# Kernel tuning notes

Hardware: AMD Instinct MI355X
Metric: run time of the kernel (lower is better)

## Reference

```python
import jax, jax.numpy as jnp
import numpy as np

HIDDEN = 128
HEADS = 4
S = 128          # number of scenes
N = 64           # pedestrians per scene
TOTAL = S * N


def setup_inputs() -> dict:
    key = jax.random.key(0)
    ks = jax.random.split(key, 12)
    h = HIDDEN
    return {
        "node_features": jax.random.normal(ks[0], (TOTAL, h), jnp.float32),
        "positions": jax.random.normal(ks[1], (TOTAL, 2), jnp.float32),
        # rel_pos_encoder: Linear(2, h//2) -> ReLU -> Linear(h//2, h)
        "W1": jax.random.normal(ks[2], (h // 2, 2), jnp.float32) * 0.5,
        "b1": jax.random.normal(ks[3], (h // 2,), jnp.float32) * 0.02,
        "W2": jax.random.normal(ks[4], (h, h // 2), jnp.float32) * (1.0 / np.sqrt(h // 2)),
        "b2": jax.random.normal(ks[5], (h,), jnp.float32) * 0.02,
        # MultiheadAttention packed in-projection (q,k,v stacked) and out-projection
        "in_proj_w": jax.random.normal(ks[6], (3 * h, h), jnp.float32) * (1.0 / np.sqrt(h)),
        "in_proj_b": jax.random.normal(ks[7], (3 * h,), jnp.float32) * 0.02,
        "out_w": jax.random.normal(ks[8], (h, h), jnp.float32) * (1.0 / np.sqrt(h)),
        "out_b": jax.random.normal(ks[9], (h,), jnp.float32) * 0.02,
        # output_proj: Linear(2h, h)
        "proj_w": jax.random.normal(ks[10], (h, 2 * h), jnp.float32) * (1.0 / np.sqrt(2 * h)),
        "proj_b": jax.random.normal(ks[11], (h,), jnp.float32) * 0.02,
        "num_scenes": S,
        "peds_per_scene": N,
    }


def reference(node_features, positions, W1, b1, W2, b2,
              in_proj_w, in_proj_b, out_w, out_b, proj_w, proj_b,
              num_scenes, peds_per_scene):
    h = node_features.shape[-1]
    heads = HEADS
    dh = h // heads
    s, n = num_scenes, peds_per_scene

    feats = node_features.reshape(s, n, h)          # (S, n, h)
    pos = positions.reshape(s, n, 2)                # (S, n, 2)

    # rel[s, i, j] = pos[j] - pos[i]  (matches unsqueeze(0) - unsqueeze(1))
    rel = pos[:, None, :, :] - pos[:, :, None, :]   # (S, n, n, 2)
    rel_enc = jnp.maximum(rel @ W1.T + b1, 0.0) @ W2.T + b2  # (S, n, n, h)

    Wq, Wk, Wv = jnp.split(in_proj_w, 3, axis=0)
    bq, bk, bv = jnp.split(in_proj_b, 3, axis=0)

    # query: each ped i attends over keys j = feats[j] + rel_enc[i, j]
    key_in = feats[:, None, :, :] + rel_enc          # (S, n, n, h)
    q = (feats @ Wq.T + bq).reshape(s, n, heads, dh)             # (S, n, H, dh)
    k = (key_in @ Wk.T + bk).reshape(s, n, n, heads, dh)         # (S, n, n, H, dh)
    v = (key_in @ Wv.T + bv).reshape(s, n, n, heads, dh)

    scores = jnp.einsum('sihd,sijhd->shij', q, k) / np.sqrt(dh)  # (S, H, n, n)
    attn = jax.nn.softmax(scores, axis=-1)
    ctx = jnp.einsum('shij,sijhd->sihd', attn, v).reshape(s, n, h)
    attn_out = ctx @ out_w.T + out_b                              # (S, n, h)

    combined = jnp.concatenate([feats, attn_out], axis=-1)       # (S, n, 2h)
    out = combined @ proj_w.T + proj_b                            # (S, n, h)
    return out.reshape(s * n, h)
```

## Files before the change

### kernel.cpp

```cpp
#include <hip/hip_runtime.h>
#include <hip/hip_bf16.h>


typedef unsigned int u32;
#define SCALE 0.17677669529663689f

__device__ __forceinline__ float bl(u32 u){ union{u32 x; float f;} c; c.x = u << 16; return c.f; }
__device__ __forceinline__ float bh(u32 u){ union{u32 x; float f;} c; c.x = u & 0xffff0000u; return c.f; }
__device__ __forceinline__ u32 pk(float a, float b){
  union{float f; u32 x;} ca, cb; ca.f = a; cb.f = b;
  u32 ua = (ca.x + 0x7fffu + ((ca.x >> 16) & 1u)) >> 16;
  u32 ub = (cb.x + 0x7fffu + ((cb.x >> 16) & 1u)) >> 16;
  return ua | (ub << 16);
}
__device__ __forceinline__ float dot8(uint4 u, float4 f0, float4 f1, float acc){
  acc = fmaf(bl(u.x), f0.x, acc); acc = fmaf(bh(u.x), f0.y, acc);
  acc = fmaf(bl(u.y), f0.z, acc); acc = fmaf(bh(u.y), f0.w, acc);
  acc = fmaf(bl(u.z), f1.x, acc); acc = fmaf(bh(u.z), f1.y, acc);
  acc = fmaf(bl(u.w), f1.z, acc); acc = fmaf(bh(u.w), f1.w, acc);
  return acc;
}
__device__ __forceinline__ void wsync(){
  __builtin_amdgcn_s_waitcnt(0xC07F);
  __builtin_amdgcn_wave_barrier();
}

__global__ __launch_bounds__(256, 2) void ee_setup(
    const float* __restrict__ nf, const float* __restrict__ b2,
    const float* __restrict__ ipw, const float* __restrict__ ipb,
    const float* __restrict__ w2,
    const float* __restrict__ ow, const float* __restrict__ pw,
    float* __restrict__ W2KT, float* __restrict__ W2VT,
    u32* __restrict__ WQB, u32* __restrict__ OWB, u32* __restrict__ PWB,
    u32* __restrict__ KBt, u32* __restrict__ VB)
{
  const int tid = threadIdx.x, b = blockIdx.x;
  const int cg = tid >> 6, l = tid & 63;
  const float2* ipw2 = (const float2*)ipw;
  const float2* ow2  = (const float2*)ow;
  const float2* pw2  = (const float2*)pw;

  if (b >= 544) {
    for (int k = 0; k < 16; ++k) {
      int i = (b - 544) * 4096 + k * 256 + tid;
      if (i < 8192)       { float2 f = ipw2[i];        WQB[i]        = pk(f.x, f.y); }
      else if (i < 16384) { float2 f = ow2[i - 8192];  OWB[i - 8192] = pk(f.x, f.y); }
      else                { float2 f = pw2[i - 16384]; PWB[i - 16384]= pk(f.x, f.y); }
    }
    return;
  }
  if (b >= 512) {
    int t = (b - 512) * 4 + cg;
    int kv = t & 1, e = t >> 1;
    int c0 = 2 * l;
    const float4* rp = (const float4*)ipw + (size_t)(128 + kv * 128 + c0) * 32;
    const float* w2e = w2 + __builtin_amdgcn_readfirstlane(e);
    float a0 = 0.f, a1 = 0.f;
    #pragma unroll 8
    for (int c4 = 0; c4 < 32; ++c4) {
      float4 wa = rp[c4], wb = rp[32 + c4];
      float x0 = w2e[(4 * c4 + 0) * 64];
      float x1 = w2e[(4 * c4 + 1) * 64];
      float x2 = w2e[(4 * c4 + 2) * 64];
      float x3 = w2e[(4 * c4 + 3) * 64];
      a0 = fmaf(wa.x, x0, a0); a0 = fmaf(wa.y, x1, a0);
      a0 = fmaf(wa.z, x2, a0); a0 = fmaf(wa.w, x3, a0);
      a1 = fmaf(wb.x, x0, a1); a1 = fmaf(wb.y, x1, a1);
      a1 = fmaf(wb.z, x2, a1); a1 = fmaf(wb.w, x3, a1);
    }
    float* dst = kv ? W2VT : W2KT;
    ((float2*)dst)[e * 64 + l] = make_float2(a0, a1);
    return;
  }

  const int s = b >> 2, kv = (b >> 1) & 1, hlf = b & 1;
  __shared__ __align__(16) u32 fbS[64][68];
  __shared__ u32 vtS[64][33];
  const float2* nf2 = (const float2*)nf;
  const float2* b22 = (const float2*)b2;

  for (int idx = tid; idx < 4096; idx += 256) {
    int j = idx >> 6, mw = idx & 63;
    float2 f = nf2[((s << 6) + j) * 64 + mw];
    float2 bb = b22[mw];
    fbS[j][mw] = pk(f.x + bb.x, f.y + bb.y);
  }
  __syncthreads();

  uint4 fr[16];
  {
    const uint4* frow = (const uint4*)&fbS[l][0];
    #pragma unroll
    for (int k = 0; k < 16; ++k) fr[k] = frow[k];
  }
  #pragma unroll 1
  for (int p = 0; p < 8; ++p) {
    int c0 = hlf * 64 + cg * 16 + 2 * p;
    int r0 = 128 + kv * 128 + c0;
    const float4* w0 = (const float4*)ipw +
                       (size_t)__builtin_amdgcn_readfirstlane(r0) * 32;
    const float4* w1r = w0 + 32;
    float a0 = ipb[r0], a1 = ipb[r0 + 1];
    #pragma unroll
    for (int k = 0; k < 16; ++k) {
      uint4 F = fr[k];
      float4 wa = w0[2 * k],  wb = w0[2 * k + 1];
      float4 xa = w1r[2 * k], xb = w1r[2 * k + 1];
      float e0 = bl(F.x), e1 = bh(F.x), e2 = bl(F.y), e3 = bh(F.y);
      float e4 = bl(F.z), e5 = bh(F.z), e6 = bl(F.w), e7 = bh(F.w);
      a0 = fmaf(e0, wa.x, a0); a0 = fmaf(e1, wa.y, a0);
      a0 = fmaf(e2, wa.z, a0); a0 = fmaf(e3, wa.w, a0);
      a0 = fmaf(e4, wb.x, a0); a0 = fmaf(e5, wb.y, a0);
      a0 = fmaf(e6, wb.z, a0); a0 = fmaf(e7, wb.w, a0);
      a1 = fmaf(e0, xa.x, a1); a1 = fmaf(e1, xa.y, a1);
      a1 = fmaf(e2, xa.z, a1); a1 = fmaf(e3, xa.w, a1);
      a1 = fmaf(e4, xb.x, a1); a1 = fmaf(e5, xb.y, a1);
      a1 = fmaf(e6, xb.z, a1); a1 = fmaf(e7, xb.w, a1);
    }
    u32 v = pk(a0, a1);
    int cw = hlf * 32 + cg * 8 + p;
    if (kv == 0) KBt[(((s << 6) + cw) << 6) + l] = v;
    else         vtS[l][cg * 8 + p] = v;
  }
  if (kv == 1) {
    __syncthreads();
    int r = tid >> 2, cb = (tid & 3) * 8;
    #pragma unroll
    for (int k = 0; k < 8; ++k)
      VB[(((s << 6) + r) << 6) + hlf * 32 + cb + k] = vtS[r][cb + k];
  }
}

__global__ __launch_bounds__(256, 2) void ee_main(
    const float* __restrict__ nf, const float* __restrict__ pos,
    const float* __restrict__ w1, const float* __restrict__ b1,
    const float* __restrict__ ipb,
    const float* __restrict__ ob, const float* __restrict__ pb,
    const float* __restrict__ W2KT, const float* __restrict__ W2VT,
    const u32* __restrict__ WQB, const u32* __restrict__ OWB,
    const u32* __restrict__ PWB,
    const u32* __restrict__ KBt, const u32* __restrict__ VB,
    float* __restrict__ outp)
{
  __shared__ __align__(16) float pxS[64], pyS[64], w1xS[64], w1yS[64], b1S[64];
  __shared__ __align__(16) float fqS[4][4][132];
  __shared__ __align__(16) float qS [4][4][132];
  __shared__ __align__(16) float qwS[4][4][4][68];
  __shared__ __align__(16) float atS[4][4][4][68];
  __shared__ __align__(16) float whS[4][4][4][68];

  const int tid = threadIdx.x;
  const int s = blockIdx.x >> 2, qt = blockIdx.x & 3;
  const int w = tid >> 6, l = tid & 63;
  const int c0 = 2 * l;

  if (tid < 64) {
    float2 p = ((const float2*)pos)[(s << 6) + tid];
    pxS[tid] = p.x; pyS[tid] = p.y;
    float2 wv = ((const float2*)w1)[tid];
    w1xS[tid] = wv.x; w1yS[tid] = wv.y;
    b1S[tid] = b1[tid];
  }
  __syncthreads();

  int il[4], ig[4];
  #pragma unroll
  for (int t = 0; t < 4; ++t) { il[t] = qt * 16 + 4 * w + t; ig[t] = (s << 6) + il[t]; }

  #pragma unroll
  for (int t = 0; t < 4; ++t)
    *(float2*)&fqS[w][t][c0] = ((const float2*)nf)[ig[t] * 64 + l];
  wsync();

  {
    float2 bq = ((const float2*)ipb)[l];
    float a0[4], a1[4];
    #pragma unroll
    for (int t = 0; t < 4; ++t) { a0[t] = bq.x; a1[t] = bq.y; }
    const uint4* W4 = (const uint4*)WQB;
    #pragma unroll 4
    for (int m8 = 0; m8 < 16; ++m8) {
      uint4 ua = W4[c0 * 16 + m8];
      uint4 ub = W4[(c0 + 1) * 16 + m8];
      #pragma unroll
      for (int t = 0; t < 4; ++t) {
        float4 f0 = *(const float4*)&fqS[w][t][8 * m8];
        float4 f1 = *(const float4*)&fqS[w][t][8 * m8 + 4];
        a0[t] = dot8(ua, f0, f1, a0[t]);
        a1[t] = dot8(ub, f0, f1, a1[t]);
      }
    }
    #pragma unroll
    for (int t = 0; t < 4; ++t)
      *(float2*)&qS[w][t][c0] = make_float2(a0[t], a1[t]);
  }
  wsync();

  {
    const float4* G4 = (const float4*)W2KT;
    #pragma unroll
    for (int hd = 0; hd < 4; ++hd) {
      float acc[4] = {0.f, 0.f, 0.f, 0.f};
      #pragma unroll
      for (int dq = 0; dq < 8; ++dq) {
        float4 g = G4[l * 32 + hd * 8 + dq];
        #pragma unroll
        for (int t = 0; t < 4; ++t) {
          float4 qf = *(const float4*)&qS[w][t][hd * 32 + 4 * dq];
          acc[t] = fmaf(g.x, qf.x, acc[t]); acc[t] = fmaf(g.y, qf.y, acc[t]);
          acc[t] = fmaf(g.z, qf.z, acc[t]); acc[t] = fmaf(g.w, qf.w, acc[t]);
        }
      }
      #pragma unroll
      for (int t = 0; t < 4; ++t) qwS[w][t][hd][l] = acc[t];
    }
  }
  wsync();

  float at[4][4];
  float pix[4], piy[4];
  {
    float pjx = pxS[l], pjy = pyS[l];
    float rx[4], ry[4];
    #pragma unroll
    for (int t = 0; t < 4; ++t) {
      pix[t] = pxS[il[t]]; piy[t] = pyS[il[t]];
      rx[t] = pjx - pix[t]; ry[t] = pjy - piy[t];
    }
    float sc[4][4];
    #pragma unroll
    for (int t = 0; t < 4; ++t)
      #pragma unroll
      for (int hd = 0; hd < 4; ++hd) sc[t][hd] = 0.f;

    const u32* kbp = KBt + (s << 12);
    #pragma unroll 8
    for (int m2 = 0; m2 < 32; ++m2) {
      u32 u0 = kbp[((2 * m2) << 6) + l];
      u32 u1 = kbp[((2 * m2 + 1) << 6) + l];
      const int hd = m2 >> 3;
      #pragma unroll
      for (int t = 0; t < 4; ++t) {
        float4 qf = *(const float4*)&qS[w][t][4 * m2];
        sc[t][hd] = fmaf(bl(u0), qf.x, sc[t][hd]);
        sc[t][hd] = fmaf(bh(u0), qf.y, sc[t][hd]);
        sc[t][hd] = fmaf(bl(u1), qf.z, sc[t][hd]);
        sc[t][hd] = fmaf(bh(u1), qf.w, sc[t][hd]);
      }
    }
    #pragma unroll 2
    for (int eb = 0; eb < 8; ++eb) {
      float4 wx0 = *(const float4*)&w1xS[8 * eb];
      float4 wx1 = *(const float4*)&w1xS[8 * eb + 4];
      float4 wy0 = *(const float4*)&w1yS[8 * eb];
      float4 wy1 = *(const float4*)&w1yS[8 * eb + 4];
      float4 bb0 = *(const float4*)&b1S[8 * eb];
      float4 bb1 = *(const float4*)&b1S[8 * eb + 4];
      #pragma unroll
      for (int t = 0; t < 4; ++t) {
        float h0 = fmaxf(0.f, fmaf(rx[t], wx0.x, fmaf(ry[t], wy0.x, bb0.x)));
        float h1 = fmaxf(0.f, fmaf(rx[t], wx0.y, fmaf(ry[t], wy0.y, bb0.y)));
        float h2 = fmaxf(0.f, fmaf(rx[t], wx0.z, fmaf(ry[t], wy0.z, bb0.z)));
        float h3 = fmaxf(0.f, fmaf(rx[t], wx0.w, fmaf(ry[t], wy0.w, bb0.w)));
        float h4 = fmaxf(0.f, fmaf(rx[t], wx1.x, fmaf(ry[t], wy1.x, bb1.x)));
        float h5 = fmaxf(0.f, fmaf(rx[t], wx1.y, fmaf(ry[t], wy1.y, bb1.y)));
        float h6 = fmaxf(0.f, fmaf(rx[t], wx1.z, fmaf(ry[t], wy1.z, bb1.z)));
        float h7 = fmaxf(0.f, fmaf(rx[t], wx1.w, fmaf(ry[t], wy1.w, bb1.w)));
        #pragma unroll
        for (int hd = 0; hd < 4; ++hd) {
          float4 q0 = *(const float4*)&qwS[w][t][hd][8 * eb];
          float4 q1 = *(const float4*)&qwS[w][t][hd][8 * eb + 4];
          float a = sc[t][hd];
          a = fmaf(q0.x, h0, a); a = fmaf(q0.y, h1, a);
          a = fmaf(q0.z, h2, a); a = fmaf(q0.w, h3, a);
          a = fmaf(q1.x, h4, a); a = fmaf(q1.y, h5, a);
          a = fmaf(q1.z, h6, a); a = fmaf(q1.w, h7, a);
          sc[t][hd] = a;
        }
      }
    }
    #pragma unroll
    for (int t = 0; t < 4; ++t) {
      #pragma unroll
      for (int hd = 0; hd < 4; ++hd) {
        float v = sc[t][hd] * SCALE;
        float m = v;
        #pragma unroll
        for (int off = 32; off > 0; off >>= 1) m = fmaxf(m, __shfl_xor(m, off));
        float p = __expf(v - m);
        float su = p;
        #pragma unroll
        for (int off = 32; off > 0; off >>= 1) su += __shfl_xor(su, off);
#if __has_builtin(__builtin_amdgcn_rcpf)
        at[t][hd] = p * __builtin_amdgcn_rcpf(su);
#else
        at[t][hd] = p / su;
#endif
        atS[w][t][hd][l] = at[t][hd];
      }
    }
  }
  wsync();

  {
    float wx = w1xS[l], wy = w1yS[l], bb = b1S[l];
    float wh[4][4];
    #pragma unroll
    for (int t = 0; t < 4; ++t)
      #pragma unroll
      for (int hd = 0; hd < 4; ++hd) wh[t][hd] = 0.f;
    #pragma unroll 4
    for (int j4 = 0; j4 < 16; ++j4) {
      float4 px = *(const float4*)&pxS[4 * j4];
      float4 py = *(const float4*)&pyS[4 * j4];
      #pragma unroll
      for (int t = 0; t < 4; ++t) {
        float4 a0v = *(const float4*)&atS[w][t][0][4 * j4];
        float4 a1v = *(const float4*)&atS[w][t][1][4 * j4];
        float4 a2v = *(const float4*)&atS[w][t][2][4 * j4];
        float4 a3v = *(const float4*)&atS[w][t][3][4 * j4];
        float h;
        h = fmaxf(0.f, fmaf(px.x - pix[t], wx, fmaf(py.x - piy[t], wy, bb)));
        wh[t][0] = fmaf(a0v.x, h, wh[t][0]); wh[t][1] = fmaf(a1v.x, h, wh[t][1]);
        wh[t][2] = fmaf(a2v.x, h, wh[t][2]); wh[t][3] = fmaf(a3v.x, h, wh[t][3]);
        h = fmaxf(0.f, fmaf(px.y - pix[t], wx, fmaf(py.y - piy[t], wy, bb)));
        wh[t][0] = fmaf(a0v.y, h, wh[t][0]); wh[t][1] = fmaf(a1v.y, h, wh[t][1]);
        wh[t][2] = fmaf(a2v.y, h, wh[t][2]); wh[t][3] = fmaf(a3v.y, h, wh[t][3]);
        h = fmaxf(0.f, fmaf(px.z - pix[t], wx, fmaf(py.z - piy[t], wy, bb)));
        wh[t][0] = fmaf(a0v.z, h, wh[t][0]); wh[t][1] = fmaf(a1v.z, h, wh[t][1]);
        wh[t][2] = fmaf(a2v.z, h, wh[t][2]); wh[t][3] = fmaf(a3v.z, h, wh[t][3]);
        h = fmaxf(0.f, fmaf(px.w - pix[t], wx, fmaf(py.w - piy[t], wy, bb)));
        wh[t][0] = fmaf(a0v.w, h, wh[t][0]); wh[t][1] = fmaf(a1v.w, h, wh[t][1]);
        wh[t][2] = fmaf(a2v.w, h, wh[t][2]); wh[t][3] = fmaf(a3v.w, h, wh[t][3]);
      }
    }
    #pragma unroll
    for (int t = 0; t < 4; ++t)
      #pragma unroll
      for (int hd = 0; hd < 4; ++hd) whS[w][t][hd][l] = wh[t][hd];
  }
  wsync();

  {
    const int hd = l >> 4;
    float cx0[4] = {0,0,0,0}, cx1[4] = {0,0,0,0};
    const float2* V2 = (const float2*)W2VT;
    const u32* vbp = VB + (s << 12);
    #pragma unroll 4
    for (int n4 = 0; n4 < 16; ++n4) {
      float2 g0 = V2[((4 * n4 + 0) << 6) + l];
      float2 g1 = V2[((4 * n4 + 1) << 6) + l];
      float2 g2 = V2[((4 * n4 + 2) << 6) + l];
      float2 g3 = V2[((4 * n4 + 3) << 6) + l];
      u32 v0 = vbp[((4 * n4 + 0) << 6) + l];
      u32 v1 = vbp[((4 * n4 + 1) << 6) + l];
      u32 v2 = vbp[((4 * n4 + 2) << 6) + l];
      u32 v3 = vbp[((4 * n4 + 3) << 6) + l];
      #pragma unroll
      for (int t = 0; t < 4; ++t) {
        float4 whv = *(const float4*)&whS[w][t][hd][4 * n4];
        float4 atv = *(const float4*)&atS[w][t][hd][4 * n4];
        float a0 = cx0[t], a1 = cx1[t];
        a0 = fmaf(whv.x, g0.x, a0); a1 = fmaf(whv.x, g0.y, a1);
        a0 = fmaf(atv.x, bl(v0), a0); a1 = fmaf(atv.x, bh(v0), a1);
        a0 = fmaf(whv.y, g1.x, a0); a1 = fmaf(whv.y, g1.y, a1);
        a0 = fmaf(atv.y, bl(v1), a0); a1 = fmaf(atv.y, bh(v1), a1);
        a0 = fmaf(whv.z, g2.x, a0); a1 = fmaf(whv.z, g2.y, a1);
        a0 = fmaf(atv.z, bl(v2), a0); a1 = fmaf(atv.z, bh(v2), a1);
        a0 = fmaf(whv.w, g3.x, a0); a1 = fmaf(whv.w, g3.y, a1);
        a0 = fmaf(atv.w, bl(v3), a0); a1 = fmaf(atv.w, bh(v3), a1);
        cx0[t] = a0; cx1[t] = a1;
      }
    }
    wsync();
    #pragma unroll
    for (int t = 0; t < 4; ++t)
      *(float2*)&qS[w][t][c0] = make_float2(cx0[t], cx1[t]);
  }
  wsync();

  {
    float2 b = ((const float2*)ob)[l];
    float a0[4], a1[4];
    #pragma unroll
    for (int t = 0; t < 4; ++t) { a0[t] = b.x; a1[t] = b.y; }
    const uint4* W4 = (const uint4*)OWB;
    #pragma unroll 4
    for (int m8 = 0; m8 < 16; ++m8) {
      uint4 ua = W4[c0 * 16 + m8];
      uint4 ub = W4[(c0 + 1) * 16 + m8];
      #pragma unroll
      for (int t = 0; t < 4; ++t) {
        float4 f0 = *(const float4*)&qS[w][t][8 * m8];
        float4 f1 = *(const float4*)&qS[w][t][8 * m8 + 4];
        a0[t] = dot8(ua, f0, f1, a0[t]);
        a1[t] = dot8(ub, f0, f1, a1[t]);
      }
    }
    wsync();
    #pragma unroll
    for (int t = 0; t < 4; ++t)
      *(float2*)(&whS[w][t][0][0] + c0) = make_float2(a0[t], a1[t]);
  }
  wsync();

  {
    float2 b = ((const float2*)pb)[l];
    float a0[4], a1[4];
    #pragma unroll
    for (int t = 0; t < 4; ++t) { a0[t] = b.x; a1[t] = b.y; }
    const uint4* W4 = (const uint4*)PWB;
    #pragma unroll 2
    for (int m8 = 0; m8 < 16; ++m8) {
      uint4 ua = W4[c0 * 32 + m8];
      uint4 ub = W4[(c0 + 1) * 32 + m8];
      uint4 uc = W4[c0 * 32 + 16 + m8];
      uint4 ud = W4[(c0 + 1) * 32 + 16 + m8];
      #pragma unroll
      for (int t = 0; t < 4; ++t) {
        float4 f0 = *(const float4*)&fqS[w][t][8 * m8];
        float4 f1 = *(const float4*)&fqS[w][t][8 * m8 + 4];
        float4 g0 = *(const float4*)(&whS[w][t][0][0] + 8 * m8);
        float4 g1 = *(const float4*)(&whS[w][t][0][0] + 8 * m8 + 4);
        a0[t] = dot8(ua, f0, f1, a0[t]);
        a1[t] = dot8(ub, f0, f1, a1[t]);
        a0[t] = dot8(uc, g0, g1, a0[t]);
        a1[t] = dot8(ud, g0, g1, a1[t]);
      }
    }
    #pragma unroll
    for (int t = 0; t < 4; ++t)
      ((float2*)outp)[ig[t] * 64 + l] = make_float2(a0[t], a1[t]);
  }
}

extern "C" void kernel_launch(void* const* d_in, const int* in_sizes, int n_in,
                              void* d_out, int out_size, void* d_ws, size_t ws_size,
                              hipStream_t stream) {
  (void)in_sizes; (void)n_in; (void)out_size; (void)ws_size;
  const float* nf  = (const float*)d_in[0];
  const float* pos = (const float*)d_in[1];
  const float* w1  = (const float*)d_in[2];
  const float* b1  = (const float*)d_in[3];
  const float* w2  = (const float*)d_in[4];
  const float* b2  = (const float*)d_in[5];
  const float* ipw = (const float*)d_in[6];
  const float* ipb = (const float*)d_in[7];
  const float* ow  = (const float*)d_in[8];
  const float* ob  = (const float*)d_in[9];
  const float* pw  = (const float*)d_in[10];
  const float* pb  = (const float*)d_in[11];

  char* ws = (char*)d_ws;
  float* W2KT = (float*)(ws);
  float* W2VT = (float*)(ws + (32 << 10));
  u32* WQB  = (u32*)(ws + (64 << 10));
  u32* OWB  = (u32*)(ws + (96 << 10));
  u32* PWB  = (u32*)(ws + (128 << 10));
  u32* KBt  = (u32*)(ws + (192 << 10));
  u32* VB   = (u32*)(ws + (192 << 10) + (128 * 4096 * 4));

  ee_setup<<<dim3(552), dim3(256), 0, stream>>>(nf, b2, ipw, ipb, w2, ow, pw,
                                                W2KT, W2VT, WQB, OWB, PWB, KBt, VB);
  ee_main<<<dim3(512), dim3(256), 0, stream>>>(nf, pos, w1, b1, ipb, ob, pb,
                                               W2KT, W2VT, WQB, OWB, PWB,
                                               KBt, VB, (float*)d_out);
}
```

Baseline: 174.5 us.

## Move Q projection and feature half of output projection into setup kernel

The setup kernel now also computes the Q projection (fp32, stored to a workspace buffer) and the node-feature half of the output projection (written directly into the output as a partial sum), doubling its per-scene block count. The main kernel drops its Q GEMV and the feature half of the final projection, reading Q from global memory and accumulating onto the partial output. This shortens the main kernel's serial chain but adds global traffic for Q and the partial result, plus more setup blocks.

```diff
diff --git a/kernel.cpp b/kernel.cpp
--- a/kernel.cpp
+++ b/kernel.cpp
@@ -29,28 +29,32 @@
     const float* __restrict__ nf, const float* __restrict__ b2,
     const float* __restrict__ ipw, const float* __restrict__ ipb,
     const float* __restrict__ w2,
-    const float* __restrict__ ow, const float* __restrict__ pw,
+    const float* __restrict__ pw, const float* __restrict__ pb,
+    const float* __restrict__ ow,
     float* __restrict__ W2KT, float* __restrict__ W2VT,
-    u32* __restrict__ WQB, u32* __restrict__ OWB, u32* __restrict__ PWB,
-    u32* __restrict__ KBt, u32* __restrict__ VB)
+    u32* __restrict__ OWB, u32* __restrict__ PW2B,
+    u32* __restrict__ KBt, u32* __restrict__ VB,
+    float* __restrict__ QB, float* __restrict__ PF)
 {
   const int tid = threadIdx.x, b = blockIdx.x;
   const int cg = tid >> 6, l = tid & 63;
-  const float2* ipw2 = (const float2*)ipw;
-  const float2* ow2  = (const float2*)ow;
-  const float2* pw2  = (const float2*)pw;
-
-  if (b >= 544) {
+
+  if (b >= 1056) {
+    const float2* ow2 = (const float2*)ow;
+    const float2* pw2 = (const float2*)pw;
     for (int k = 0; k < 16; ++k) {
-      int i = (b - 544) * 4096 + k * 256 + tid;
-      if (i < 8192)       { float2 f = ipw2[i];        WQB[i]        = pk(f.x, f.y); }
-      else if (i < 16384) { float2 f = ow2[i - 8192];  OWB[i - 8192] = pk(f.x, f.y); }
-      else                { float2 f = pw2[i - 16384]; PWB[i - 16384]= pk(f.x, f.y); }
+      int i = (b - 1056) * 4096 + k * 256 + tid;
+      if (i < 8192) { float2 f = ow2[i]; OWB[i] = pk(f.x, f.y); }
+      else {
+        int m = i - 8192; int c = m >> 6, mw = m & 63;
+        float2 f = pw2[c * 128 + 64 + mw];
+        PW2B[m] = pk(f.x, f.y);
+      }
     }
     return;
   }
-  if (b >= 512) {
-    int t = (b - 512) * 4 + cg;
+  if (b >= 1024) {
+    int t = (b - 1024) * 4 + cg;
     int kv = t & 1, e = t >> 1;
     int c0 = 2 * l;
     const float4* rp = (const float4*)ipw + (size_t)(128 + kv * 128 + c0) * 32;
@@ -73,17 +77,17 @@
     return;
   }
 
-  const int s = b >> 2, kv = (b >> 1) & 1, hlf = b & 1;
+  const int s = b >> 3, mat = (b >> 1) & 3, hlf = b & 1;
   __shared__ __align__(16) u32 fbS[64][68];
-  __shared__ u32 vtS[64][33];
+  __shared__ __align__(16) u32 xS[64][68];
   const float2* nf2 = (const float2*)nf;
   const float2* b22 = (const float2*)b2;
 
   for (int idx = tid; idx < 4096; idx += 256) {
     int j = idx >> 6, mw = idx & 63;
     float2 f = nf2[((s << 6) + j) * 64 + mw];
-    float2 bb = b22[mw];
-    fbS[j][mw] = pk(f.x + bb.x, f.y + bb.y);
+    if (mat < 2) { float2 bb = b22[mw]; f.x += bb.x; f.y += bb.y; }
+    fbS[j][mw] = pk(f.x, f.y);
   }
   __syncthreads();
 
@@ -93,14 +97,18 @@
     #pragma unroll
     for (int k = 0; k < 16; ++k) fr[k] = frow[k];
   }
+  const float* wbase = (mat == 3) ? pw : ipw;
+  const int rbase = (mat == 0) ? 128 : (mat == 1) ? 256 : 0;
+  const int rlen4 = (mat == 3) ? 64 : 32;
+  const float* bptr = (mat == 3) ? pb : (ipb + rbase);
+
   #pragma unroll 1
   for (int p = 0; p < 8; ++p) {
     int c0 = hlf * 64 + cg * 16 + 2 * p;
-    int r0 = 128 + kv * 128 + c0;
-    const float4* w0 = (const float4*)ipw +
-                       (size_t)__builtin_amdgcn_readfirstlane(r0) * 32;
-    const float4* w1r = w0 + 32;
-    float a0 = ipb[r0], a1 = ipb[r0 + 1];
+    int row = __builtin_amdgcn_readfirstlane(rbase + c0);
+    const float4* w0 = (const float4*)wbase + (size_t)row * rlen4;
+    const float4* w1r = w0 + rlen4;
+    float a0 = bptr[c0], a1 = bptr[c0 + 1];
     #pragma unroll
     for (int k = 0; k < 16; ++k) {
       uint4 F = fr[k];
@@ -117,37 +125,48 @@
       a1 = fmaf(e4, xb.x, a1); a1 = fmaf(e5, xb.y, a1);
       a1 = fmaf(e6, xb.z, a1); a1 = fmaf(e7, xb.w, a1);
     }
-    u32 v = pk(a0, a1);
-    int cw = hlf * 32 + cg * 8 + p;
-    if (kv == 0) KBt[(((s << 6) + cw) << 6) + l] = v;
-    else         vtS[l][cg * 8 + p] = v;
-  }
-  if (kv == 1) {
+    if (mat == 0) {
+      KBt[(((s << 6) + hlf * 32 + cg * 8 + p) << 6) + l] = pk(a0, a1);
+    } else if (mat == 1) {
+      xS[l][cg * 8 + p] = pk(a0, a1);
+    } else {
+      float* fx = (float*)xS;
+      fx[l * 68 + cg * 16 + 2 * p]     = a0;
+      fx[l * 68 + cg * 16 + 2 * p + 1] = a1;
+    }
+  }
+  if (mat == 1) {
     __syncthreads();
     int r = tid >> 2, cb = (tid & 3) * 8;
     #pragma unroll
     for (int k = 0; k < 8; ++k)
-      VB[(((s << 6) + r) << 6) + hlf * 32 + cb + k] = vtS[r][cb + k];
+      VB[(((s << 6) + r) << 6) + hlf * 32 + cb + k] = xS[r][cb + k];
+  } else if (mat >= 2) {
+    __syncthreads();
+    int r = tid >> 2, g = (tid & 3) * 16;
+    const float* fx = (const float*)xS;
+    float* dst = (mat == 2) ? QB : PF;
+    #pragma unroll
+    for (int k = 0; k < 16; ++k)
+      dst[((s << 6) + r) * 128 + hlf * 64 + g + k] = fx[r * 68 + g + k];
   }
 }
 
 __global__ __launch_bounds__(256, 2) void ee_main(
-    const float* __restrict__ nf, const float* __restrict__ pos,
+    const float* __restrict__ pos,
     const float* __restrict__ w1, const float* __restrict__ b1,
-    const float* __restrict__ ipb,
-    const float* __restrict__ ob, const float* __restrict__ pb,
+    const float* __restrict__ ob,
     const float* __restrict__ W2KT, const float* __restrict__ W2VT,
-    const u32* __restrict__ WQB, const u32* __restrict__ OWB,
-    const u32* __restrict__ PWB,
+    const u32* __restrict__ OWB, const u32* __restrict__ PW2B,
     const u32* __restrict__ KBt, const u32* __restrict__ VB,
+    const float* __restrict__ QB,
     float* __restrict__ outp)
 {
   __shared__ __align__(16) float pxS[64], pyS[64], w1xS[64], w1yS[64], b1S[64];
-  __shared__ __align__(16) float fqS[4][4][132];
-  __shared__ __align__(16) float qS [4][4][132];
   __shared__ __align__(16) float qwS[4][4][4][68];
   __shared__ __align__(16) float atS[4][4][4][68];
   __shared__ __align__(16) float whS[4][4][4][68];
+  __shared__ __align__(16) float cxS[4][4][132];
 
   const int tid = threadIdx.x;
   const int s = blockIdx.x >> 2, qt = blockIdx.x & 3;
@@ -163,38 +182,15 @@
   }
   __syncthreads();
 
+  const int wq = __builtin_amdgcn_readfirstlane(w);
   int il[4], ig[4];
+  const float4* q4[4];
   #pragma unroll
-  for (int t = 0; t < 4; ++t) { il[t] = qt * 16 + 4 * w + t; ig[t] = (s << 6) + il[t]; }
-
-  #pragma unroll
-  for (int t = 0; t < 4; ++t)
-    *(float2*)&fqS[w][t][c0] = ((const float2*)nf)[ig[t] * 64 + l];
-  wsync();
-
-  {
-    float2 bq = ((const float2*)ipb)[l];
-    float a0[4], a1[4];
-    #pragma unroll
-    for (int t = 0; t < 4; ++t) { a0[t] = bq.x; a1[t] = bq.y; }
-    const uint4* W4 = (const uint4*)WQB;
-    #pragma unroll 4
-    for (int m8 = 0; m8 < 16; ++m8) {
-      uint4 ua = W4[c0 * 16 + m8];
-      uint4 ub = W4[(c0 + 1) * 16 + m8];
-      #pragma unroll
-      for (int t = 0; t < 4; ++t) {
-        float4 f0 = *(const float4*)&fqS[w][t][8 * m8];
-        float4 f1 = *(const float4*)&fqS[w][t][8 * m8 + 4];
-        a0[t] = dot8(ua, f0, f1, a0[t]);
-        a1[t] = dot8(ub, f0, f1, a1[t]);
-      }
-    }
-    #pragma unroll
-    for (int t = 0; t < 4; ++t)
-      *(float2*)&qS[w][t][c0] = make_float2(a0[t], a1[t]);
-  }
-  wsync();
+  for (int t = 0; t < 4; ++t) {
+    il[t] = qt * 16 + 4 * wq + t;
+    ig[t] = (s << 6) + il[t];
+    q4[t] = (const float4*)(QB + (size_t)ig[t] * 128);
+  }
 
   {
     const float4* G4 = (const float4*)W2KT;
@@ -206,7 +202,7 @@
         float4 g = G4[l * 32 + hd * 8 + dq];
         #pragma unroll
         for (int t = 0; t < 4; ++t) {
-          float4 qf = *(const float4*)&qS[w][t][hd * 32 + 4 * dq];
+          float4 qf = q4[t][hd * 8 + dq];
           acc[t] = fmaf(g.x, qf.x, acc[t]); acc[t] = fmaf(g.y, qf.y, acc[t]);
           acc[t] = fmaf(g.z, qf.z, acc[t]); acc[t] = fmaf(g.w, qf.w, acc[t]);
         }
@@ -239,13 +235,14 @@
       u32 u0 = kbp[((2 * m2) << 6) + l];
       u32 u1 = kbp[((2 * m2 + 1) << 6) + l];
       const int hd = m2 >> 3;
-      #pragma unroll
-      for (int t = 0; t < 4; ++t) {
-        float4 qf = *(const float4*)&qS[w][t][4 * m2];
-        sc[t][hd] = fmaf(bl(u0), qf.x, sc[t][hd]);
-        sc[t][hd] = fmaf(bh(u0), qf.y, sc[t][hd]);
-        sc[t][hd] = fmaf(bl(u1), qf.z, sc[t][hd]);
-        sc[t][hd] = fmaf(bh(u1), qf.w, sc[t][hd]);
+      float f0 = bl(u0), f1 = bh(u0), f2 = bl(u1), f3 = bh(u1);
+      #pragma unroll
+      for (int t = 0; t < 4; ++t) {
+        float4 qf = q4[t][m2];
+        sc[t][hd] = fmaf(f0, qf.x, sc[t][hd]);
+        sc[t][hd] = fmaf(f1, qf.y, sc[t][hd]);
+        sc[t][hd] = fmaf(f2, qf.z, sc[t][hd]);
+        sc[t][hd] = fmaf(f3, qf.w, sc[t][hd]);
       }
     }
     #pragma unroll 2
@@ -372,10 +369,9 @@
         cx0[t] = a0; cx1[t] = a1;
       }
     }
-    wsync();
-    #pragma unroll
-    for (int t = 0; t < 4; ++t)
-      *(float2*)&qS[w][t][c0] = make_float2(cx0[t], cx1[t]);
+    #pragma unroll
+    for (int t = 0; t < 4; ++t)
+      *(float2*)&cxS[w][t][c0] = make_float2(cx0[t], cx1[t]);
   }
   wsync();
 
@@ -391,8 +387,8 @@
       uint4 ub = W4[(c0 + 1) * 16 + m8];
       #pragma unroll
       for (int t = 0; t < 4; ++t) {
-        float4 f0 = *(const float4*)&qS[w][t][8 * m8];
-        float4 f1 = *(const float4*)&qS[w][t][8 * m8 + 4];
+        float4 f0 = *(const float4*)&cxS[w][t][8 * m8];
+        float4 f1 = *(const float4*)&cxS[w][t][8 * m8 + 4];
         a0[t] = dot8(ua, f0, f1, a0[t]);
         a1[t] = dot8(ub, f0, f1, a1[t]);
       }
@@ -400,32 +396,28 @@
     wsync();
     #pragma unroll
     for (int t = 0; t < 4; ++t)
-      *(float2*)(&whS[w][t][0][0] + c0) = make_float2(a0[t], a1[t]);
+      *(float2*)&cxS[w][t][c0] = make_float2(a0[t], a1[t]);
   }
   wsync();
 
   {
-    float2 b = ((const float2*)pb)[l];
     float a0[4], a1[4];
     #pragma unroll
-    for (int t = 0; t < 4; ++t) { a0[t] = b.x; a1[t] = b.y; }
-    const uint4* W4 = (const uint4*)PWB;
-    #pragma unroll 2
+    for (int t = 0; t < 4; ++t) {
+      float2 pf = ((const float2*)outp)[ig[t] * 64 + l];
+      a0[t] = pf.x; a1[t] = pf.y;
+    }
+    const uint4* W4 = (const uint4*)PW2B;
+    #pragma unroll 4
     for (int m8 = 0; m8 < 16; ++m8) {
-      uint4 ua = W4[c0 * 32 + m8];
-      uint4 ub = W4[(c0 + 1) * 32 + m8];
-      uint4 uc = W4[c0 * 32 + 16 + m8];
-      uint4 ud = W4[(c0 + 1) * 32 + 16 + m8];
-      #pragma unroll
-      for (int t = 0; t < 4; ++t) {
-        float4 f0 = *(const float4*)&fqS[w][t][8 * m8];
-        float4 f1 = *(const float4*)&fqS[w][t][8 * m8 + 4];
-        float4 g0 = *(const float4*)(&whS[w][t][0][0] + 8 * m8);
-        float4 g1 = *(const float4*)(&whS[w][t][0][0] + 8 * m8 + 4);
+      uint4 ua = W4[c0 * 16 + m8];
+      uint4 ub = W4[(c0 + 1) * 16 + m8];
+      #pragma unroll
+      for (int t = 0; t < 4; ++t) {
+        float4 f0 = *(const float4*)&cxS[w][t][8 * m8];
+        float4 f1 = *(const float4*)&cxS[w][t][8 * m8 + 4];
         a0[t] = dot8(ua, f0, f1, a0[t]);
         a1[t] = dot8(ub, f0, f1, a1[t]);
-        a0[t] = dot8(uc, g0, g1, a0[t]);
-        a1[t] = dot8(ud, g0, g1, a1[t]);
       }
     }
     #pragma unroll
@@ -454,15 +446,17 @@
   char* ws = (char*)d_ws;
   float* W2KT = (float*)(ws);
   float* W2VT = (float*)(ws + (32 << 10));
-  u32* WQB  = (u32*)(ws + (64 << 10));
-  u32* OWB  = (u32*)(ws + (96 << 10));
-  u32* PWB  = (u32*)(ws + (128 << 10));
-  u32* KBt  = (u32*)(ws + (192 << 10));
-  u32* VB   = (u32*)(ws + (192 << 10) + (128 * 4096 * 4));
-
-  ee_setup<<<dim3(552), dim3(256), 0, stream>>>(nf, b2, ipw, ipb, w2, ow, pw,
-                                                W2KT, W2VT, WQB, OWB, PWB, KBt, VB);
-  ee_main<<<dim3(512), dim3(256), 0, stream>>>(nf, pos, w1, b1, ipb, ob, pb,
-                                               W2KT, W2VT, WQB, OWB, PWB,
-                                               KBt, VB, (float*)d_out);
-}
+  u32* OWB   = (u32*)(ws + (64 << 10));
+  u32* PW2B  = (u32*)(ws + (96 << 10));
+  u32* KBt   = (u32*)(ws + (128 << 10));
+  u32* VB    = (u32*)(ws + (128 << 10) + (128 * 4096 * 4));
+  float* QB  = (float*)(ws + (128 << 10) + (2 * 128 * 4096 * 4));
+  float* PF  = (float*)d_out;
+
+  ee_setup<<<dim3(1060), dim3(256), 0, stream>>>(nf, b2, ipw, ipb, w2, pw, pb, ow,
+                                                 W2KT, W2VT, OWB, PW2B,
+                                                 KBt, VB, QB, PF);
+  ee_main<<<dim3(512), dim3(256), 0, stream>>>(pos, w1, b1, ob,
+                                               W2KT, W2VT, OWB, PW2B,
+                                               KBt, VB, QB, (float*)d_out);
+}
```

New measurement: 224.6 us. 28.7% more time.

## Halve queries per wave, broadcast q via readlane, shrink LDS for higher occupancy

Applied to the files above, without the earlier changes.

ee_main now handles 2 query rows per wave instead of 4 and launches 1024 blocks. Per-row vectors (q, context, attention output) stay in registers and are broadcast with readlane instead of round-tripping through shared memory. The shared-memory footprint shrinks to two small scratch arrays and launch bounds rise to 4 blocks per CU, aiming for more parallelism and fewer LDS syncs. The trade-off is that weight loads are amortized over fewer rows, and many readlane scalar ops are added; W2KT is also stored transposed by the setup kernel to match the new access pattern.

```diff
diff --git a/kernel.cpp b/kernel.cpp
--- a/kernel.cpp
+++ b/kernel.cpp
@@ -20,6 +20,21 @@
   acc = fmaf(bl(u.w), f1.z, acc); acc = fmaf(bh(u.w), f1.w, acc);
   return acc;
 }
+__device__ __forceinline__ float dot8v(uint4 u, const float* x, float acc){
+  acc = fmaf(bl(u.x), x[0], acc); acc = fmaf(bh(u.x), x[1], acc);
+  acc = fmaf(bl(u.y), x[2], acc); acc = fmaf(bh(u.y), x[3], acc);
+  acc = fmaf(bl(u.z), x[4], acc); acc = fmaf(bh(u.z), x[5], acc);
+  acc = fmaf(bl(u.w), x[6], acc); acc = fmaf(bh(u.w), x[7], acc);
+  return acc;
+}
+__device__ __forceinline__ float rl(float v, int lane){
+  return __int_as_float(__builtin_amdgcn_readlane(__float_as_int(v), lane));
+}
+#define RL8(dst, r0, r1, base4) \
+  dst[0] = rl(r0, (base4));     dst[1] = rl(r1, (base4)); \
+  dst[2] = rl(r0, (base4) + 1); dst[3] = rl(r1, (base4) + 1); \
+  dst[4] = rl(r0, (base4) + 2); dst[5] = rl(r1, (base4) + 2); \
+  dst[6] = rl(r0, (base4) + 3); dst[7] = rl(r1, (base4) + 3);
 __device__ __forceinline__ void wsync(){
   __builtin_amdgcn_s_waitcnt(0xC07F);
   __builtin_amdgcn_wave_barrier();
@@ -68,8 +83,11 @@
       a1 = fmaf(wb.x, x0, a1); a1 = fmaf(wb.y, x1, a1);
       a1 = fmaf(wb.z, x2, a1); a1 = fmaf(wb.w, x3, a1);
     }
-    float* dst = kv ? W2VT : W2KT;
-    ((float2*)dst)[e * 64 + l] = make_float2(a0, a1);
+    if (kv) ((float2*)W2VT)[e * 64 + l] = make_float2(a0, a1);
+    else {
+      W2KT[(2 * l) * 64 + e]     = a0;
+      W2KT[(2 * l + 1) * 64 + e] = a1;
+    }
     return;
   }
 
@@ -131,11 +149,11 @@
   }
 }
 
-__global__ __launch_bounds__(256, 2) void ee_main(
+__global__ __launch_bounds__(256, 4) void ee_main(
     const float* __restrict__ nf, const float* __restrict__ pos,
     const float* __restrict__ w1, const float* __restrict__ b1,
-    const float* __restrict__ ipb,
-    const float* __restrict__ ob, const float* __restrict__ pb,
+    const float* __restrict__ ipb, const float* __restrict__ ob,
+    const float* __restrict__ pb,
     const float* __restrict__ W2KT, const float* __restrict__ W2VT,
     const u32* __restrict__ WQB, const u32* __restrict__ OWB,
     const u32* __restrict__ PWB,
@@ -143,14 +161,11 @@
     float* __restrict__ outp)
 {
   __shared__ __align__(16) float pxS[64], pyS[64], w1xS[64], w1yS[64], b1S[64];
-  __shared__ __align__(16) float fqS[4][4][132];
-  __shared__ __align__(16) float qS [4][4][132];
-  __shared__ __align__(16) float qwS[4][4][4][68];
-  __shared__ __align__(16) float atS[4][4][4][68];
-  __shared__ __align__(16) float whS[4][4][4][68];
+  __shared__ __align__(16) float scrS[4][2][4][68];
+  __shared__ __align__(16) float atS [4][2][4][68];
 
   const int tid = threadIdx.x;
-  const int s = blockIdx.x >> 2, qt = blockIdx.x & 3;
+  const int s = blockIdx.x >> 3, qo = blockIdx.x & 7;
   const int w = tid >> 6, l = tid & 63;
   const int c0 = 2 * l;
 
@@ -163,89 +178,88 @@
   }
   __syncthreads();
 
-  int il[4], ig[4];
+  int il[2], ig[2];
+  const float4* fB[2];
   #pragma unroll
-  for (int t = 0; t < 4; ++t) { il[t] = qt * 16 + 4 * w + t; ig[t] = (s << 6) + il[t]; }
-
-  #pragma unroll
-  for (int t = 0; t < 4; ++t)
-    *(float2*)&fqS[w][t][c0] = ((const float2*)nf)[ig[t] * 64 + l];
-  wsync();
-
+  for (int t = 0; t < 2; ++t) {
+    il[t] = qo * 8 + 2 * w + t;
+    ig[t] = (s << 6) + il[t];
+    fB[t] = (const float4*)nf +
+            (size_t)__builtin_amdgcn_readfirstlane(ig[t]) * 32;
+  }
+
+  float q0r[2], q1r[2];
   {
     float2 bq = ((const float2*)ipb)[l];
-    float a0[4], a1[4];
-    #pragma unroll
-    for (int t = 0; t < 4; ++t) { a0[t] = bq.x; a1[t] = bq.y; }
+    float a0[2] = {bq.x, bq.x}, a1[2] = {bq.y, bq.y};
     const uint4* W4 = (const uint4*)WQB;
     #pragma unroll 4
     for (int m8 = 0; m8 < 16; ++m8) {
       uint4 ua = W4[c0 * 16 + m8];
       uint4 ub = W4[(c0 + 1) * 16 + m8];
       #pragma unroll
-      for (int t = 0; t < 4; ++t) {
-        float4 f0 = *(const float4*)&fqS[w][t][8 * m8];
-        float4 f1 = *(const float4*)&fqS[w][t][8 * m8 + 4];
+      for (int t = 0; t < 2; ++t) {
+        float4 f0 = fB[t][2 * m8], f1 = fB[t][2 * m8 + 1];
         a0[t] = dot8(ua, f0, f1, a0[t]);
         a1[t] = dot8(ub, f0, f1, a1[t]);
       }
     }
-    #pragma unroll
-    for (int t = 0; t < 4; ++t)
-      *(float2*)&qS[w][t][c0] = make_float2(a0[t], a1[t]);
+    q0r[0] = a0[0]; q0r[1] = a0[1]; q1r[0] = a1[0]; q1r[1] = a1[1];
+  }
+
+  {
+    float acc[2][4];
+    #pragma unroll
+    for (int t = 0; t < 2; ++t)
+      #pragma unroll
+      for (int hd = 0; hd < 4; ++hd) acc[t][hd] = 0.f;
+    #pragma unroll
+    for (int ch2 = 0; ch2 < 64; ++ch2) {
+      float g0 = W2KT[(2 * ch2) * 64 + l];
+      float g1 = W2KT[(2 * ch2 + 1) * 64 + l];
+      const int hd = ch2 >> 4;
+      #pragma unroll
+      for (int t = 0; t < 2; ++t) {
+        acc[t][hd] = fmaf(g0, rl(q0r[t], ch2), acc[t][hd]);
+        acc[t][hd] = fmaf(g1, rl(q1r[t], ch2), acc[t][hd]);
+      }
+    }
+    #pragma unroll
+    for (int t = 0; t < 2; ++t)
+      #pragma unroll
+      for (int hd = 0; hd < 4; ++hd) scrS[w][t][hd][l] = acc[t][hd];
   }
   wsync();
 
-  {
-    const float4* G4 = (const float4*)W2KT;
-    #pragma unroll
-    for (int hd = 0; hd < 4; ++hd) {
-      float acc[4] = {0.f, 0.f, 0.f, 0.f};
-      #pragma unroll
-      for (int dq = 0; dq < 8; ++dq) {
-        float4 g = G4[l * 32 + hd * 8 + dq];
-        #pragma unroll
-        for (int t = 0; t < 4; ++t) {
-          float4 qf = *(const float4*)&qS[w][t][hd * 32 + 4 * dq];
-          acc[t] = fmaf(g.x, qf.x, acc[t]); acc[t] = fmaf(g.y, qf.y, acc[t]);
-          acc[t] = fmaf(g.z, qf.z, acc[t]); acc[t] = fmaf(g.w, qf.w, acc[t]);
-        }
-      }
-      #pragma unroll
-      for (int t = 0; t < 4; ++t) qwS[w][t][hd][l] = acc[t];
-    }
-  }
-  wsync();
-
-  float at[4][4];
-  float pix[4], piy[4];
+  float at_[2][4];
+  float pix[2], piy[2];
   {
     float pjx = pxS[l], pjy = pyS[l];
-    float rx[4], ry[4];
-    #pragma unroll
-    for (int t = 0; t < 4; ++t) {
+    float rx[2], ry[2];
+    #pragma unroll
+    for (int t = 0; t < 2; ++t) {
       pix[t] = pxS[il[t]]; piy[t] = pyS[il[t]];
       rx[t] = pjx - pix[t]; ry[t] = pjy - piy[t];
     }
-    float sc[4][4];
-    #pragma unroll
-    for (int t = 0; t < 4; ++t)
+    float sc[2][4];
+    #pragma unroll
+    for (int t = 0; t < 2; ++t)
       #pragma unroll
       for (int hd = 0; hd < 4; ++hd) sc[t][hd] = 0.f;
 
     const u32* kbp = KBt + (s << 12);
-    #pragma unroll 8
+    #pragma unroll
     for (int m2 = 0; m2 < 32; ++m2) {
       u32 u0 = kbp[((2 * m2) << 6) + l];
       u32 u1 = kbp[((2 * m2 + 1) << 6) + l];
       const int hd = m2 >> 3;
-      #pragma unroll
-      for (int t = 0; t < 4; ++t) {
-        float4 qf = *(const float4*)&qS[w][t][4 * m2];
-        sc[t][hd] = fmaf(bl(u0), qf.x, sc[t][hd]);
-        sc[t][hd] = fmaf(bh(u0), qf.y, sc[t][hd]);
-        sc[t][hd] = fmaf(bl(u1), qf.z, sc[t][hd]);
-        sc[t][hd] = fmaf(bh(u1), qf.w, sc[t][hd]);
+      float k0 = bl(u0), k1 = bh(u0), k2 = bl(u1), k3 = bh(u1);
+      #pragma unroll
+      for (int t = 0; t < 2; ++t) {
+        sc[t][hd] = fmaf(k0, rl(q0r[t], 2 * m2),     sc[t][hd]);
+        sc[t][hd] = fmaf(k1, rl(q1r[t], 2 * m2),     sc[t][hd]);
+        sc[t][hd] = fmaf(k2, rl(q0r[t], 2 * m2 + 1), sc[t][hd]);
+        sc[t][hd] = fmaf(k3, rl(q1r[t], 2 * m2 + 1), sc[t][hd]);
       }
     }
     #pragma unroll 2
@@ -257,7 +271,7 @@
       float4 bb0 = *(const float4*)&b1S[8 * eb];
       float4 bb1 = *(const float4*)&b1S[8 * eb + 4];
       #pragma unroll
-      for (int t = 0; t < 4; ++t) {
+      for (int t = 0; t < 2; ++t) {
         float h0 = fmaxf(0.f, fmaf(rx[t], wx0.x, fmaf(ry[t], wy0.x, bb0.x)));
         float h1 = fmaxf(0.f, fmaf(rx[t], wx0.y, fmaf(ry[t], wy0.y, bb0.y)));
         float h2 = fmaxf(0.f, fmaf(rx[t], wx0.z, fmaf(ry[t], wy0.z, bb0.z)));
@@ -268,19 +282,19 @@
         float h7 = fmaxf(0.f, fmaf(rx[t], wx1.w, fmaf(ry[t], wy1.w, bb1.w)));
         #pragma unroll
         for (int hd = 0; hd < 4; ++hd) {
-          float4 q0 = *(const float4*)&qwS[w][t][hd][8 * eb];
-          float4 q1 = *(const float4*)&qwS[w][t][hd][8 * eb + 4];
+          float4 g0 = *(const float4*)&scrS[w][t][hd][8 * eb];
+          float4 g1 = *(const float4*)&scrS[w][t][hd][8 * eb + 4];
           float a = sc[t][hd];
-          a = fmaf(q0.x, h0, a); a = fmaf(q0.y, h1, a);
-          a = fmaf(q0.z, h2, a); a = fmaf(q0.w, h3, a);
-          a = fmaf(q1.x, h4, a); a = fmaf(q1.y, h5, a);
-          a = fmaf(q1.z, h6, a); a = fmaf(q1.w, h7, a);
+          a = fmaf(g0.x, h0, a); a = fmaf(g0.y, h1, a);
+          a = fmaf(g0.z, h2, a); a = fmaf(g0.w, h3, a);
+          a = fmaf(g1.x, h4, a); a = fmaf(g1.y, h5, a);
+          a = fmaf(g1.z, h6, a); a = fmaf(g1.w, h7, a);
           sc[t][hd] = a;
         }
       }
     }
     #pragma unroll
-    for (int t = 0; t < 4; ++t) {
+    for (int t = 0; t < 2; ++t) {
       #pragma unroll
       for (int hd = 0; hd < 4; ++hd) {
         float v = sc[t][hd] * SCALE;
@@ -292,11 +306,11 @@
         #pragma unroll
         for (int off = 32; off > 0; off >>= 1) su += __shfl_xor(su, off);
 #if __has_builtin(__builtin_amdgcn_rcpf)
-        at[t][hd] = p * __builtin_amdgcn_rcpf(su);
+        at_[t][hd] = p * __builtin_amdgcn_rcpf(su);
 #else
-        at[t][hd] = p / su;
+        at_[t][hd] = p / su;
 #endif
-        atS[w][t][hd][l] = at[t][hd];
+        atS[w][t][hd][l] = at_[t][hd];
       }
     }
   }
@@ -304,9 +318,9 @@
 
   {
     float wx = w1xS[l], wy = w1yS[l], bb = b1S[l];
-    float wh[4][4];
-    #pragma unroll
-    for (int t = 0; t < 4; ++t)
+    float wh[2][4];
+    #pragma unroll
+    for (int t = 0; t < 2; ++t)
       #pragma unroll
       for (int hd = 0; hd < 4; ++hd) wh[t][hd] = 0.f;
     #pragma unroll 4
@@ -314,7 +328,7 @@
       float4 px = *(const float4*)&pxS[4 * j4];
       float4 py = *(const float4*)&pyS[4 * j4];
       #pragma unroll
-      for (int t = 0; t < 4; ++t) {
+      for (int t = 0; t < 2; ++t) {
         float4 a0v = *(const float4*)&atS[w][t][0][4 * j4];
         float4 a1v = *(const float4*)&atS[w][t][1][4 * j4];
         float4 a2v = *(const float4*)&atS[w][t][2][4 * j4];
@@ -335,15 +349,15 @@
       }
     }
     #pragma unroll
-    for (int t = 0; t < 4; ++t)
-      #pragma unroll
-      for (int hd = 0; hd < 4; ++hd) whS[w][t][hd][l] = wh[t][hd];
+    for (int t = 0; t < 2; ++t)
+      #pragma unroll
+      for (int hd = 0; hd < 4; ++hd) scrS[w][t][hd][l] = wh[t][hd];
   }
   wsync();
 
+  float cx0[2] = {0.f, 0.f}, cx1[2] = {0.f, 0.f};
   {
     const int hd = l >> 4;
-    float cx0[4] = {0,0,0,0}, cx1[4] = {0,0,0,0};
     const float2* V2 = (const float2*)W2VT;
     const u32* vbp = VB + (s << 12);
     #pragma unroll 4
@@ -357,8 +371,8 @@
       u32 v2 = vbp[((4 * n4 + 2) << 6) + l];
       u32 v3 = vbp[((4 * n4 + 3) << 6) + l];
       #pragma unroll
-      for (int t = 0; t < 4; ++t) {
-        float4 whv = *(const float4*)&whS[w][t][hd][4 * n4];
+      for (int t = 0; t < 2; ++t) {
+        float4 whv = *(const float4*)&scrS[w][t][hd][4 * n4];
         float4 atv = *(const float4*)&atS[w][t][hd][4 * n4];
         float a0 = cx0[t], a1 = cx1[t];
         a0 = fmaf(whv.x, g0.x, a0); a1 = fmaf(whv.x, g0.y, a1);
@@ -372,64 +386,57 @@
         cx0[t] = a0; cx1[t] = a1;
       }
     }
-    wsync();
-    #pragma unroll
-    for (int t = 0; t < 4; ++t)
-      *(float2*)&qS[w][t][c0] = make_float2(cx0[t], cx1[t]);
-  }
-  wsync();
-
+  }
+
+  float ao0[2], ao1[2];
   {
     float2 b = ((const float2*)ob)[l];
-    float a0[4], a1[4];
-    #pragma unroll
-    for (int t = 0; t < 4; ++t) { a0[t] = b.x; a1[t] = b.y; }
+    float a0[2] = {b.x, b.x}, a1[2] = {b.y, b.y};
     const uint4* W4 = (const uint4*)OWB;
     #pragma unroll 4
     for (int m8 = 0; m8 < 16; ++m8) {
       uint4 ua = W4[c0 * 16 + m8];
       uint4 ub = W4[(c0 + 1) * 16 + m8];
       #pragma unroll
-      for (int t = 0; t < 4; ++t) {
-        float4 f0 = *(const float4*)&qS[w][t][8 * m8];
-        float4 f1 = *(const float4*)&qS[w][t][8 * m8 + 4];
+      for (int t = 0; t < 2; ++t) {
+        float x[8];
+        RL8(x, cx0[t], cx1[t], 4 * m8)
+        a0[t] = dot8v(ua, x, a0[t]);
+        a1[t] = dot8v(ub, x, a1[t]);
+      }
+    }
+    ao0[0] = a0[0]; ao0[1] = a0[1]; ao1[0] = a1[0]; ao1[1] = a1[1];
+  }
+
+  {
+    float2 b = ((const float2*)pb)[l];
+    float a0[2] = {b.x, b.x}, a1[2] = {b.y, b.y};
+    const uint4* W4 = (const uint4*)PWB;
+    #pragma unroll 4
+    for (int g = 0; g < 16; ++g) {
+      uint4 ua = W4[c0 * 32 + g];
+      uint4 ub = W4[(c0 + 1) * 32 + g];
+      #pragma unroll
+      for (int t = 0; t < 2; ++t) {
+        float4 f0 = fB[t][2 * g], f1 = fB[t][2 * g + 1];
         a0[t] = dot8(ua, f0, f1, a0[t]);
         a1[t] = dot8(ub, f0, f1, a1[t]);
       }
     }
-    wsync();
-    #pragma unroll
-    for (int t = 0; t < 4; ++t)
-      *(float2*)(&whS[w][t][0][0] + c0) = make_float2(a0[t], a1[t]);
-  }
-  wsync();
-
-  {
-    float2 b = ((const float2*)pb)[l];
-    float a0[4], a1[4];
-    #pragma unroll
-    for (int t = 0; t < 4; ++t) { a0[t] = b.x; a1[t] = b.y; }
-    const uint4* W4 = (const uint4*)PWB;
-    #pragma unroll 2
-    for (int m8 = 0; m8 < 16; ++m8) {
-      uint4 ua = W4[c0 * 32 + m8];
-      uint4 ub = W4[(c0 + 1) * 32 + m8];
-      uint4 uc = W4[c0 * 32 + 16 + m8];
-      uint4 ud = W4[(c0 + 1) * 32 + 16 + m8];
-      #pragma unroll
-      for (int t = 0; t < 4; ++t) {
-        float4 f0 = *(const float4*)&fqS[w][t][8 * m8];
-        float4 f1 = *(const float4*)&fqS[w][t][8 * m8 + 4];
-        float4 g0 = *(const float4*)(&whS[w][t][0][0] + 8 * m8);
-        float4 g1 = *(const float4*)(&whS[w][t][0][0] + 8 * m8 + 4);
-        a0[t] = dot8(ua, f0, f1, a0[t]);
-        a1[t] = dot8(ub, f0, f1, a1[t]);
-        a0[t] = dot8(uc, g0, g1, a0[t]);
-        a1[t] = dot8(ud, g0, g1, a1[t]);
-      }
-    }
-    #pragma unroll
-    for (int t = 0; t < 4; ++t)
+    #pragma unroll 4
+    for (int g = 0; g < 16; ++g) {
+      uint4 ua = W4[c0 * 32 + 16 + g];
+      uint4 ub = W4[(c0 + 1) * 32 + 16 + g];
+      #pragma unroll
+      for (int t = 0; t < 2; ++t) {
+        float x[8];
+        RL8(x, ao0[t], ao1[t], 4 * g)
+        a0[t] = dot8v(ua, x, a0[t]);
+        a1[t] = dot8v(ub, x, a1[t]);
+      }
+    }
+    #pragma unroll
+    for (int t = 0; t < 2; ++t)
       ((float2*)outp)[ig[t] * 64 + l] = make_float2(a0[t], a1[t]);
   }
 }
@@ -462,7 +469,7 @@
 
   ee_setup<<<dim3(552), dim3(256), 0, stream>>>(nf, b2, ipw, ipb, w2, ow, pw,
                                                 W2KT, W2VT, WQB, OWB, PWB, KBt, VB);
-  ee_main<<<dim3(512), dim3(256), 0, stream>>>(nf, pos, w1, b1, ipb, ob, pb,
-                                               W2KT, W2VT, WQB, OWB, PWB,
-                                               KBt, VB, (float*)d_out);
-}
+  ee_main<<<dim3(1024), dim3(256), 0, stream>>>(nf, pos, w1, b1, ipb, ob, pb,
+                                                W2KT, W2VT, WQB, OWB, PWB,
+                                                KBt, VB, (float*)d_out);
+}
```

Result: slower. 222.0 us (+27.2%).
